# Performance work log

Measured on AMD Instinct MI355X. Metric: run time of the kernel, lower is better.

## Reference

```python
import jax, jax.numpy as jnp
import numpy as np

B, S, D_IN, D_OUT = 4, 4096, 768, 64


def setup_inputs() -> dict:
    key = jax.random.key(0)
    kx, kq, kk, kv = jax.random.split(key, 4)
    x = jax.random.normal(kx, (B, S, D_IN), dtype=jnp.float32)
    # kaiming-uniform-ish scale for weights
    bound = 1.0 / np.sqrt(D_IN)
    Wq = jax.random.uniform(kq, (D_IN, D_OUT), jnp.float32, -bound, bound)
    Wk = jax.random.uniform(kk, (D_IN, D_OUT), jnp.float32, -bound, bound)
    Wv = jax.random.uniform(kv, (D_IN, D_OUT), jnp.float32, -bound, bound)
    return {"x": x, "Wq": Wq, "Wk": Wk, "Wv": Wv}


def reference(x, Wq, Wk, Wv):
    # QKV projections (qkv_bias=False)
    q = jnp.einsum("bsi,io->bso", x, Wq)  # [B,S,D_OUT]
    k = jnp.einsum("bsi,io->bso", x, Wk)
    v = jnp.einsum("bsi,io->bso", x, Wv)
    # scores [B,S,S], causal mask (upper triangle excl. diag -> -inf)
    scores = jnp.einsum("bqd,bkd->bqk", q, k)
    num_tokens = x.shape[1]
    causal = jnp.triu(jnp.ones((num_tokens, num_tokens), dtype=bool), k=1)
    scores = jnp.where(causal[None, :, :], -jnp.inf, scores)
    scale = 1.0 / np.sqrt(k.shape[-1]).astype(np.float32)
    attn = jax.nn.softmax(scores * scale, axis=-1)
    # dropout: eval mode -> identity (module's custom Dropout is a no-op when not training)
    ctx = jnp.einsum("bqk,bkv->bqv", attn, v)  # [B,S,D_OUT]
    return ctx
```

## Files before the change

kernel.cpp:

```cpp
#include <hip/hip_runtime.h>
#include <stdint.h>

#define KSTEPS 24
#define TOKENS 16384

typedef short short8 __attribute__((ext_vector_type(8)));
typedef float fx4 __attribute__((ext_vector_type(4)));
typedef unsigned short u16;
typedef u16 u16x4 __attribute__((ext_vector_type(4)));

static __device__ __forceinline__ u16 f2bf(float f) {
  union { float f; unsigned u; } v; v.f = f;
  return (u16)((v.u + 0x7fffu + ((v.u >> 16) & 1u)) >> 16);
}

static __device__ __forceinline__ u16 p2bf(float f) {
  union { float f; unsigned u; } v; v.f = f;
  return (u16)((v.u + 0x8000u) >> 16);
}

static __device__ __forceinline__ fx4 mfma16(short8 a, short8 b, fx4 c) {
  return __builtin_amdgcn_mfma_f32_16x16x32_bf16(a, b, c, 0, 0, 0);
}

static __device__ __forceinline__ void async16(const void* g, void* l) {
  __builtin_amdgcn_global_load_lds(
      (const __attribute__((address_space(1))) void*)g,
      (__attribute__((address_space(3))) void*)(unsigned int)(uintptr_t)l,
      16, 0, 0);
}

__global__ void prep_w_kernel(const float* __restrict__ Wq, const float* __restrict__ Wk,
                              const float* __restrict__ Wv, u16* __restrict__ wfrag) {
  int idx  = blockIdx.x * 256 + threadIdx.x;
  int lane = idx & 63;
  int fid  = idx >> 6;
  int nt   = fid & 3;
  int ks   = (fid >> 2) % KSTEPS;
  int mat  = fid / (KSTEPS * 4);
  const float* W = (mat == 0) ? Wq : (mat == 1) ? Wk : Wv;
  int n  = nt * 16 + (lane & 15);
  int k0 = ks * 32 + (lane >> 4) * 8;
  short8 out;
#pragma unroll
  for (int j = 0; j < 8; j++) out[j] = (short)f2bf(W[(size_t)(k0 + j) * 64 + n]);
  *(short8*)(wfrag + (size_t)idx * 8) = out;
}

__global__ __launch_bounds__(256) void proj_kernel(const float* __restrict__ x,
                                                   const u16* __restrict__ wfrag,
                                                   u16* __restrict__ qb,
                                                   u16* __restrict__ kb,
                                                   u16* __restrict__ vT) {
  __shared__ float xs[2][32 * 32];
  __shared__ u16  Ws[2][12 * 512];

  int w = threadIdx.x >> 6, lane = threadIdx.x & 63;
  int ln = lane & 15, quad = lane >> 4;
  int rw = w >> 1, cs = w & 1;
  int s0 = blockIdx.x * 32;

  fx4 acc[6];
#pragma unroll
  for (int j = 0; j < 6; j++) acc[j] = (fx4){0.f, 0.f, 0.f, 0.f};

  int srow  = w * 8 + (lane >> 3);
  int slot  = lane & 7;
  int chunk = slot ^ (srow & 7);
  const float* xsrc = x + (size_t)(s0 + srow) * 768 + chunk * 4;

#pragma unroll
  for (int m = 0; m < 3; m++)
    async16(wfrag + ((size_t)(m * KSTEPS + 0) * 256 + w * 64 + lane) * 8,
            (char*)Ws[0] + m * 4096 + w * 1024 + lane * 16);
  async16(xsrc, (char*)xs[0] + w * 1024 + lane * 16);

  int r = rw * 16 + ln;
  for (int ks = 0; ks < KSTEPS; ks++) {
    __syncthreads();
    if (ks < KSTEPS - 1) {
      int buf = (ks + 1) & 1;
#pragma unroll
      for (int m = 0; m < 3; m++)
        async16(wfrag + ((size_t)(m * KSTEPS + ks + 1) * 256 + w * 64 + lane) * 8,
                (char*)Ws[buf] + m * 4096 + w * 1024 + lane * 16);
      async16(xsrc + (ks + 1) * 32, (char*)xs[buf] + w * 1024 + lane * 16);
    }
    const float* xb = xs[ks & 1];
    const u16*  wb = Ws[ks & 1];
    int sl0 = (2 * quad)     ^ (r & 7);
    int sl1 = (2 * quad + 1) ^ (r & 7);
    fx4 xa = *(const fx4*)(xb + r * 32 + sl0 * 4);
    fx4 xv = *(const fx4*)(xb + r * 32 + sl1 * 4);
    short8 af;
#pragma unroll
    for (int j = 0; j < 4; j++) { af[j] = (short)f2bf(xa[j]); af[4 + j] = (short)f2bf(xv[j]); }
#pragma unroll
    for (int j = 0; j < 6; j++) {
      short8 bf = *(const short8*)(wb + (cs * 6 + j) * 512 + lane * 8);
      acc[j] = mfma16(af, bf, acc[j]);
    }
  }

  int tok0 = s0 + rw * 16 + quad * 4;
#pragma unroll
  for (int j = 0; j < 6; j++) {
    int f = cs * 6 + j;
    int d = (f & 3) * 16 + ln;
    if (f < 4) {
#pragma unroll
      for (int reg = 0; reg < 4; reg++)
        qb[(size_t)(tok0 + reg) * 64 + d] = f2bf(acc[j][reg] * 0.180336887f);
    } else if (f < 8) {
#pragma unroll
      for (int reg = 0; reg < 4; reg++)
        kb[(size_t)(tok0 + reg) * 64 + d] = f2bf(acc[j][reg]);
    } else {
      int b = tok0 >> 12, s = tok0 & 4095;
      u16x4 vp;
#pragma unroll
      for (int reg = 0; reg < 4; reg++) vp[reg] = f2bf(acc[j][reg]);
      *(u16x4*)(vT + ((size_t)b * 64 + d) * 4096 + s) = vp;
    }
  }
}

__global__ __launch_bounds__(512) void attn_kernel(const u16* __restrict__ qb,
                                                   const u16* __restrict__ kb,
                                                   const u16* __restrict__ vT,
                                                   float* __restrict__ o0g,
                                                   float* __restrict__ po5,
                                                   float* __restrict__ mlb) {
  __shared__ u16 Kstg[2][4096];
  __shared__ u16 Vstg[2][4096];
  __shared__ u16 Ps[8][16 * 72];

  int w = threadIdx.x >> 6, lane = threadIdx.x & 63;
  int ln = lane & 15, quad = lane >> 4;
  int band = 31 - blockIdx.x;
  int b = blockIdx.y, z = blockIdx.z;
  int q0 = band * 128;
  int qw = q0 + w * 16;

  const u16* qbb = qb + (size_t)b * 4096 * 64;
  const u16* kbb = kb + (size_t)b * 4096 * 64;
  const u16* vtb = vT + (size_t)b * 64 * 4096;

  short8 qf0 = *(const short8*)(qbb + (size_t)(qw + ln) * 64 + quad * 8);
  short8 qf1 = *(const short8*)(qbb + (size_t)(qw + ln) * 64 + 32 + quad * 8);

  short8 ones;
#pragma unroll
  for (int j = 0; j < 8; j++) ones[j] = (short)0x3F80;

  fx4 o[4];
#pragma unroll
  for (int nt2 = 0; nt2 < 4; nt2++) o[nt2] = (fx4){0.f, 0.f, 0.f, 0.f};
  float l_i[4] = {0.f, 0.f, 0.f, 0.f};

  int n = 2 * band + 2;
  int c = (n + 5) / 6;
  int lo = z * c; if (lo > n) lo = n;
  int hi = lo + c; if (hi > n) hi = n;

  int cc = w * 64 + lane;
  int srow = cc >> 3, sslot = cc & 7, sw_ = (sslot ^ (srow & 7)) * 8;
  if (lo < hi) {
    async16(kbb + ((size_t)lo * 64 + srow) * 64 + sw_, (char*)Kstg[0] + cc * 16);
    async16(vtb + (size_t)srow * 4096 + lo * 64 + sw_, (char*)Vstg[0] + cc * 16);
  }

  for (int t = lo; t < hi; t++) {
    __syncthreads();
    if (t + 1 < hi) {
      int nb = (t - lo + 1) & 1;
      async16(kbb + ((size_t)(t + 1) * 64 + srow) * 64 + sw_, (char*)Kstg[nb] + cc * 16);
      async16(vtb + (size_t)srow * 4096 + (t + 1) * 64 + sw_, (char*)Vstg[nb] + cc * 16);
    }
    if (64 * t > qw + 15) continue;

    const u16* Kb = Kstg[(t - lo) & 1];
    const u16* Vb = Vstg[(t - lo) & 1];

    fx4 sA[4];
#pragma unroll
    for (int nt = 0; nt < 4; nt++) {
      int row = nt * 16 + ln;
      int s0_ = quad ^ (row & 7), s1_ = (quad + 4) ^ (row & 7);
      short8 kf0 = *(const short8*)(Kb + (row * 8 + s0_) * 8);
      short8 kf1 = *(const short8*)(Kb + (row * 8 + s1_) * 8);
      sA[nt] = mfma16(qf0, kf0, (fx4){0.f, 0.f, 0.f, 0.f});
      sA[nt] = mfma16(qf1, kf1, sA[nt]);
    }

    if (64 * t + 63 > qw) {
#pragma unroll
      for (int nt = 0; nt < 4; nt++)
#pragma unroll
        for (int reg = 0; reg < 4; reg++) {
          int col = t * 64 + nt * 16 + ln;
          int rowg = qw + quad * 4 + reg;
          if (col > rowg) sA[nt][reg] = -1e30f;
        }
    }

#pragma unroll
    for (int nt = 0; nt < 4; nt++)
#pragma unroll
      for (int reg = 0; reg < 4; reg++)
        Ps[w][(quad * 4 + reg) * 72 + nt * 16 + ln] =
            p2bf(__builtin_amdgcn_exp2f(sA[nt][reg]));

    short8 pf0 = *(const short8*)(&Ps[w][ln * 72 + quad * 8]);
    short8 pf1 = *(const short8*)(&Ps[w][ln * 72 + 32 + quad * 8]);

    fx4 lacc = mfma16(pf0, ones, (fx4){0.f, 0.f, 0.f, 0.f});
    lacc = mfma16(pf1, ones, lacc);
#pragma unroll
    for (int reg = 0; reg < 4; reg++) l_i[reg] += lacc[reg];

#pragma unroll
    for (int nt2 = 0; nt2 < 4; nt2++) {
      int row = nt2 * 16 + ln;
      int s0_ = quad ^ (row & 7), s1_ = (quad + 4) ^ (row & 7);
      short8 vf0 = *(const short8*)(Vb + (row * 8 + s0_) * 8);
      short8 vf1 = *(const short8*)(Vb + (row * 8 + s1_) * 8);
      o[nt2] = mfma16(pf0, vf0, o[nt2]);
      o[nt2] = mfma16(pf1, vf1, o[nt2]);
    }
  }

  float* dst = (z == 0) ? o0g : (po5 + (size_t)(z - 1) * 4 * 4096 * 64);
#pragma unroll
  for (int nt2 = 0; nt2 < 4; nt2++)
#pragma unroll
    for (int reg = 0; reg < 4; reg++) {
      int rowg = qw + quad * 4 + reg;
      dst[((size_t)b * 4096 + rowg) * 64 + nt2 * 16 + ln] = o[nt2][reg];
    }
  if (ln == 0) {
#pragma unroll
    for (int reg = 0; reg < 4; reg++) {
      int rowg = qw + quad * 4 + reg;
      mlb[((size_t)z * 4 + b) * 4096 + rowg] = l_i[reg];
    }
  }
}

__global__ __launch_bounds__(256) void merge_kernel(float* __restrict__ out,
                                                    const float* __restrict__ po5,
                                                    const float* __restrict__ mlb) {
  int qt = blockIdx.x, b = blockIdx.y;
  int r = threadIdx.x >> 3;
  int c = (threadIdx.x & 7) * 8;
  size_t row = (size_t)b * 4096 + qt * 32 + r;
  float l = mlb[row];
#pragma unroll
  for (int z = 1; z < 6; z++) l += mlb[(size_t)z * 4 * 4096 + row];
  float inv = 1.0f / l;
  float* op = out + row * 64 + c;
  fx4 u0 = *(fx4*)op, u1 = *(fx4*)(op + 4);
#pragma unroll
  for (int z = 1; z < 6; z++) {
    const float* pp = po5 + (size_t)(z - 1) * 4 * 4096 * 64 + row * 64 + c;
    fx4 v0 = *(const fx4*)pp, v1 = *(const fx4*)(pp + 4);
#pragma unroll
    for (int j = 0; j < 4; j++) { u0[j] += v0[j]; u1[j] += v1[j]; }
  }
#pragma unroll
  for (int j = 0; j < 4; j++) { u0[j] *= inv; u1[j] *= inv; }
  *(fx4*)op = u0;
  *(fx4*)(op + 4) = u1;
}

extern "C" void kernel_launch(void* const* d_in, const int* in_sizes, int n_in,
                              void* d_out, int out_size, void* d_ws, size_t ws_size,
                              hipStream_t stream) {
  const float* x  = (const float*)d_in[0];
  const float* Wq = (const float*)d_in[1];
  const float* Wk = (const float*)d_in[2];
  const float* Wv = (const float*)d_in[3];

  u16* qbw = (u16*)d_ws;
  u16* kbw = qbw + (size_t)TOKENS * 64;
  u16* vtw = kbw + (size_t)TOKENS * 64;
  u16* wfr = vtw + (size_t)TOKENS * 64;
  float* po5 = (float*)(wfr + (size_t)3 * KSTEPS * 256 * 8);
  float* mlb = po5 + (size_t)5 * 4 * 4096 * 64;

  prep_w_kernel<<<72, 256, 0, stream>>>(Wq, Wk, Wv, wfr);
  proj_kernel<<<TOKENS / 32, 256, 0, stream>>>(x, wfr, qbw, kbw, vtw);
  attn_kernel<<<dim3(32, 4, 6), 512, 0, stream>>>(qbw, kbw, vtw,
                                                  (float*)d_out, po5, mlb);
  merge_kernel<<<dim3(128, 4), 256, 0, stream>>>((float*)d_out, po5, mlb);
}
```

Measured before the change: 138.6 us.

## Process 32 query rows per wave with 4-wave blocks to reuse K/V fragments

Halves the number of waves per attention block (8 to 4) and gives each wave two 16-row query tiles, so every K and V fragment read from LDS feeds two MFMA chains. The goal is fewer LDS reads per MFMA and fewer waves contending for the same staged tiles. The cost is higher register pressure (doubled accumulators and P fragments), coarser causal skipping per wave, and fewer waves per block to hide latency, partly offset by a launch bound of 3 blocks per CU.

After: 136.6 us. Within noise of the previous version (-1.5%).

```diff
diff --git a/kernel.cpp b/kernel.cpp
--- a/kernel.cpp
+++ b/kernel.cpp
@@ -125,72 +125,85 @@
   }
 }
 
-__global__ __launch_bounds__(512) void attn_kernel(const u16* __restrict__ qb,
-                                                   const u16* __restrict__ kb,
-                                                   const u16* __restrict__ vT,
-                                                   float* __restrict__ o0g,
-                                                   float* __restrict__ po5,
-                                                   float* __restrict__ mlb) {
+__global__ __launch_bounds__(256, 3) void attn_kernel(const u16* __restrict__ qb,
+                                                      const u16* __restrict__ kb,
+                                                      const u16* __restrict__ vT,
+                                                      float* __restrict__ o0g,
+                                                      float* __restrict__ po5,
+                                                      float* __restrict__ mlb) {
   __shared__ u16 Kstg[2][4096];
   __shared__ u16 Vstg[2][4096];
-  __shared__ u16 Ps[8][16 * 72];
+  __shared__ u16 Ps[4][32 * 72];
 
   int w = threadIdx.x >> 6, lane = threadIdx.x & 63;
   int ln = lane & 15, quad = lane >> 4;
   int band = 31 - blockIdx.x;
   int b = blockIdx.y, z = blockIdx.z;
   int q0 = band * 128;
-  int qw = q0 + w * 16;
+  int qw = q0 + w * 32;
 
   const u16* qbb = qb + (size_t)b * 4096 * 64;
   const u16* kbb = kb + (size_t)b * 4096 * 64;
   const u16* vtb = vT + (size_t)b * 64 * 4096;
 
-  short8 qf0 = *(const short8*)(qbb + (size_t)(qw + ln) * 64 + quad * 8);
-  short8 qf1 = *(const short8*)(qbb + (size_t)(qw + ln) * 64 + 32 + quad * 8);
+  short8 qf0a = *(const short8*)(qbb + (size_t)(qw + ln) * 64 + quad * 8);
+  short8 qf1a = *(const short8*)(qbb + (size_t)(qw + ln) * 64 + 32 + quad * 8);
+  short8 qf0b = *(const short8*)(qbb + (size_t)(qw + 16 + ln) * 64 + quad * 8);
+  short8 qf1b = *(const short8*)(qbb + (size_t)(qw + 16 + ln) * 64 + 32 + quad * 8);
 
   short8 ones;
 #pragma unroll
   for (int j = 0; j < 8; j++) ones[j] = (short)0x3F80;
 
-  fx4 o[4];
-#pragma unroll
-  for (int nt2 = 0; nt2 < 4; nt2++) o[nt2] = (fx4){0.f, 0.f, 0.f, 0.f};
-  float l_i[4] = {0.f, 0.f, 0.f, 0.f};
+  fx4 oa[4], ob[4];
+#pragma unroll
+  for (int j = 0; j < 4; j++) { oa[j] = (fx4){0.f,0.f,0.f,0.f}; ob[j] = (fx4){0.f,0.f,0.f,0.f}; }
+  float la[4] = {0.f,0.f,0.f,0.f}, lb[4] = {0.f,0.f,0.f,0.f};
 
   int n = 2 * band + 2;
   int c = (n + 5) / 6;
   int lo = z * c; if (lo > n) lo = n;
   int hi = lo + c; if (hi > n) hi = n;
 
-  int cc = w * 64 + lane;
-  int srow = cc >> 3, sslot = cc & 7, sw_ = (sslot ^ (srow & 7)) * 8;
+  int t0c = w * 64 + lane;
   if (lo < hi) {
-    async16(kbb + ((size_t)lo * 64 + srow) * 64 + sw_, (char*)Kstg[0] + cc * 16);
-    async16(vtb + (size_t)srow * 4096 + lo * 64 + sw_, (char*)Vstg[0] + cc * 16);
+#pragma unroll
+    for (int j = 0; j < 2; j++) {
+      int cc = t0c + j * 256;
+      int row = cc >> 3, slot = cc & 7, sw_ = (slot ^ (row & 7)) * 8;
+      async16(kbb + ((size_t)lo * 64 + row) * 64 + sw_, (char*)Kstg[0] + cc * 16);
+      async16(vtb + (size_t)row * 4096 + lo * 64 + sw_, (char*)Vstg[0] + cc * 16);
+    }
   }
 
   for (int t = lo; t < hi; t++) {
     __syncthreads();
     if (t + 1 < hi) {
       int nb = (t - lo + 1) & 1;
-      async16(kbb + ((size_t)(t + 1) * 64 + srow) * 64 + sw_, (char*)Kstg[nb] + cc * 16);
-      async16(vtb + (size_t)srow * 4096 + (t + 1) * 64 + sw_, (char*)Vstg[nb] + cc * 16);
-    }
-    if (64 * t > qw + 15) continue;
+#pragma unroll
+      for (int j = 0; j < 2; j++) {
+        int cc = t0c + j * 256;
+        int row = cc >> 3, slot = cc & 7, sw_ = (slot ^ (row & 7)) * 8;
+        async16(kbb + ((size_t)(t + 1) * 64 + row) * 64 + sw_, (char*)Kstg[nb] + cc * 16);
+        async16(vtb + (size_t)row * 4096 + (t + 1) * 64 + sw_, (char*)Vstg[nb] + cc * 16);
+      }
+    }
+    if (64 * t > qw + 31) continue;
 
     const u16* Kb = Kstg[(t - lo) & 1];
     const u16* Vb = Vstg[(t - lo) & 1];
 
-    fx4 sA[4];
+    fx4 sAa[4], sAb[4];
 #pragma unroll
     for (int nt = 0; nt < 4; nt++) {
       int row = nt * 16 + ln;
       int s0_ = quad ^ (row & 7), s1_ = (quad + 4) ^ (row & 7);
       short8 kf0 = *(const short8*)(Kb + (row * 8 + s0_) * 8);
       short8 kf1 = *(const short8*)(Kb + (row * 8 + s1_) * 8);
-      sA[nt] = mfma16(qf0, kf0, (fx4){0.f, 0.f, 0.f, 0.f});
-      sA[nt] = mfma16(qf1, kf1, sA[nt]);
+      sAa[nt] = mfma16(qf0a, kf0, (fx4){0.f,0.f,0.f,0.f});
+      sAa[nt] = mfma16(qf1a, kf1, sAa[nt]);
+      sAb[nt] = mfma16(qf0b, kf0, (fx4){0.f,0.f,0.f,0.f});
+      sAb[nt] = mfma16(qf1b, kf1, sAb[nt]);
     }
 
     if (64 * t + 63 > qw) {
@@ -199,25 +212,35 @@
 #pragma unroll
         for (int reg = 0; reg < 4; reg++) {
           int col = t * 64 + nt * 16 + ln;
-          int rowg = qw + quad * 4 + reg;
-          if (col > rowg) sA[nt][reg] = -1e30f;
+          int ra = qw + quad * 4 + reg;
+          if (col > ra) sAa[nt][reg] = -1e30f;
+          if (col > ra + 16) sAb[nt][reg] = -1e30f;
         }
     }
 
 #pragma unroll
     for (int nt = 0; nt < 4; nt++)
 #pragma unroll
-      for (int reg = 0; reg < 4; reg++)
+      for (int reg = 0; reg < 4; reg++) {
         Ps[w][(quad * 4 + reg) * 72 + nt * 16 + ln] =
-            p2bf(__builtin_amdgcn_exp2f(sA[nt][reg]));
-
-    short8 pf0 = *(const short8*)(&Ps[w][ln * 72 + quad * 8]);
-    short8 pf1 = *(const short8*)(&Ps[w][ln * 72 + 32 + quad * 8]);
-
-    fx4 lacc = mfma16(pf0, ones, (fx4){0.f, 0.f, 0.f, 0.f});
-    lacc = mfma16(pf1, ones, lacc);
-#pragma unroll
-    for (int reg = 0; reg < 4; reg++) l_i[reg] += lacc[reg];
+            p2bf(__builtin_amdgcn_exp2f(sAa[nt][reg]));
+        Ps[w][(16 + quad * 4 + reg) * 72 + nt * 16 + ln] =
+            p2bf(__builtin_amdgcn_exp2f(sAb[nt][reg]));
+      }
+
+    short8 pf0a = *(const short8*)(&Ps[w][ln * 72 + quad * 8]);
+    short8 pf1a = *(const short8*)(&Ps[w][ln * 72 + 32 + quad * 8]);
+    short8 pf0b = *(const short8*)(&Ps[w][(16 + ln) * 72 + quad * 8]);
+    short8 pf1b = *(const short8*)(&Ps[w][(16 + ln) * 72 + 32 + quad * 8]);
+
+    fx4 lacc = mfma16(pf0a, ones, (fx4){0.f,0.f,0.f,0.f});
+    lacc = mfma16(pf1a, ones, lacc);
+#pragma unroll
+    for (int reg = 0; reg < 4; reg++) la[reg] += lacc[reg];
+    lacc = mfma16(pf0b, ones, (fx4){0.f,0.f,0.f,0.f});
+    lacc = mfma16(pf1b, ones, lacc);
+#pragma unroll
+    for (int reg = 0; reg < 4; reg++) lb[reg] += lacc[reg];
 
 #pragma unroll
     for (int nt2 = 0; nt2 < 4; nt2++) {
@@ -225,8 +248,10 @@
       int s0_ = quad ^ (row & 7), s1_ = (quad + 4) ^ (row & 7);
       short8 vf0 = *(const short8*)(Vb + (row * 8 + s0_) * 8);
       short8 vf1 = *(const short8*)(Vb + (row * 8 + s1_) * 8);
-      o[nt2] = mfma16(pf0, vf0, o[nt2]);
-      o[nt2] = mfma16(pf1, vf1, o[nt2]);
+      oa[nt2] = mfma16(pf0a, vf0, oa[nt2]);
+      oa[nt2] = mfma16(pf1a, vf1, oa[nt2]);
+      ob[nt2] = mfma16(pf0b, vf0, ob[nt2]);
+      ob[nt2] = mfma16(pf1b, vf1, ob[nt2]);
     }
   }
 
@@ -235,14 +260,16 @@
   for (int nt2 = 0; nt2 < 4; nt2++)
 #pragma unroll
     for (int reg = 0; reg < 4; reg++) {
-      int rowg = qw + quad * 4 + reg;
-      dst[((size_t)b * 4096 + rowg) * 64 + nt2 * 16 + ln] = o[nt2][reg];
+      int ra = qw + quad * 4 + reg;
+      dst[((size_t)b * 4096 + ra) * 64 + nt2 * 16 + ln] = oa[nt2][reg];
+      dst[((size_t)b * 4096 + ra + 16) * 64 + nt2 * 16 + ln] = ob[nt2][reg];
     }
   if (ln == 0) {
 #pragma unroll
     for (int reg = 0; reg < 4; reg++) {
-      int rowg = qw + quad * 4 + reg;
-      mlb[((size_t)z * 4 + b) * 4096 + rowg] = l_i[reg];
+      int ra = qw + quad * 4 + reg;
+      mlb[((size_t)z * 4 + b) * 4096 + ra] = la[reg];
+      mlb[((size_t)z * 4 + b) * 4096 + ra + 16] = lb[reg];
     }
   }
 }
@@ -290,7 +317,7 @@
 
   prep_w_kernel<<<72, 256, 0, stream>>>(Wq, Wk, Wv, wfr);
   proj_kernel<<<TOKENS / 32, 256, 0, stream>>>(x, wfr, qbw, kbw, vtw);
-  attn_kernel<<<dim3(32, 4, 6), 512, 0, stream>>>(qbw, kbw, vtw,
+  attn_kernel<<<dim3(32, 4, 6), 256, 0, stream>>>(qbw, kbw, vtw,
                                                   (float*)d_out, po5, mlb);
   merge_kernel<<<dim3(128, 4), 256, 0, stream>>>((float*)d_out, po5, mlb);
 }
```
